# Kernel tuning notes

Hardware: AMD Instinct MI355X
Metric: run time of the kernel (lower is better)

## Reference

```python
import jax, jax.numpy as jnp
import numpy as np

N_NODES = 50000

def setup_inputs() -> dict:
    key = jax.random.key(0)
    ks = jax.random.split(key, 8)
    in_dim, hidden_dim, out_dim = 128, 128, 128
    n_edges = 800000
    features = jax.random.normal(ks[0], (N_NODES, in_dim), dtype=jnp.float32)
    src = jax.random.randint(ks[1], (n_edges,), 0, N_NODES, dtype=jnp.int64)
    dst = jax.random.randint(ks[2], (n_edges,), 0, N_NODES, dtype=jnp.int64)
    # nn.Linear params: weight [out,in], bias [out]
    W1 = jax.random.normal(ks[3], (hidden_dim, in_dim), dtype=jnp.float32) / np.sqrt(in_dim)
    b1 = jax.random.normal(ks[4], (hidden_dim,), dtype=jnp.float32) * 0.01
    W2 = jax.random.normal(ks[5], (out_dim, hidden_dim), dtype=jnp.float32) / np.sqrt(hidden_dim)
    b2 = jax.random.normal(ks[6], (out_dim,), dtype=jnp.float32) * 0.01
    return {"features": features, "src": src, "dst": dst,
            "W1": W1, "b1": b1, "W2": W2, "b2": b2}

def _mpnn_layer(feat, src, dst, W, b):
    # DGL copy_u + sum: message = feat[src], summed at dst nodes
    msgs = feat[src]                                  # [E, d] gather
    h_neigh = jax.ops.segment_sum(msgs, dst, num_segments=N_NODES)  # [N, d]
    return h_neigh @ W.T + b                          # dense linear

def reference(features, src, dst, W1, b1, W2, b2):
    h = _mpnn_layer(features, src, dst, W1, b1)
    h = jax.nn.relu(h)
    h = _mpnn_layer(h, src, dst, W2, b2)
    return h
```

## Files before the change

### kernel.cpp

```cpp
#include <hip/hip_runtime.h>


#define NDIM 128
#define SCAN_BS 512
#define BKT_SHIFT 8
#define BKT_NODES 256
#define TILE 4096
#define NBK_MAX 256

typedef __attribute__((ext_vector_type(8))) short bf16x8;
typedef __attribute__((ext_vector_type(4))) float f32x4;
typedef __attribute__((ext_vector_type(2))) float f32x2;

__device__ inline unsigned short f2bf_rne(float x) {
    unsigned u = __float_as_uint(x);
    unsigned lsb = (u >> 16) & 1u;
    u += 0x7fffu + lsb;
    return (unsigned short)(u >> 16);
}

__device__ inline unsigned pack_bf2(float lo, float hi) {
    return (unsigned)f2bf_rne(lo) | ((unsigned)f2bf_rne(hi) << 16);
}

__global__ __launch_bounds__(1024) void hist_convert(
        const int* __restrict__ dst, int* __restrict__ hist_g,
        int n_edges, int ntiles, int nbk,
        const float* __restrict__ feat, const float* __restrict__ W1,
        const float* __restrict__ W2,
        unsigned char* __restrict__ feat_f8,
        unsigned short* __restrict__ w1_bf,
        unsigned short* __restrict__ w2_bf, int n8) {
    __shared__ int lh[NBK_MAX];
    int t = threadIdx.x;
    if (blockIdx.x < (unsigned)ntiles) {
        int tblk = blockIdx.x;
        if (t < nbk) lh[t] = 0;
        __syncthreads();
        int e0 = tblk * TILE;
        int e1 = min(e0 + TILE, n_edges);
        for (int e = e0 + t; e < e1; e += 1024)
            atomicAdd(&lh[dst[e] >> BKT_SHIFT], 1);
        __syncthreads();
        if (t < nbk) hist_g[t * ntiles + tblk] = lh[t];
    } else {
        int i = (blockIdx.x - ntiles) * 1024 + t;
        if (i < n8) {
            const float4* p = reinterpret_cast<const float4*>(feat + (size_t)i * 8);
            float4 a = p[0], b = p[1];
            int w0 = __builtin_amdgcn_cvt_pk_fp8_f32(a.x, a.y, 0, false);
            w0 = __builtin_amdgcn_cvt_pk_fp8_f32(a.z, a.w, w0, true);
            int w1 = __builtin_amdgcn_cvt_pk_fp8_f32(b.x, b.y, 0, false);
            w1 = __builtin_amdgcn_cvt_pk_fp8_f32(b.z, b.w, w1, true);
            uint2 pk; pk.x = (unsigned)w0; pk.y = (unsigned)w1;
            *reinterpret_cast<uint2*>(feat_f8 + (size_t)i * 8) = pk;
        } else if (i < n8 + 4096) {
            int j = i - n8;
            const float* srcp = (j < 2048) ? W1 : W2;
            unsigned short* dstp = (j < 2048) ? w1_bf : w2_bf;
            int jj = j & 2047;
            const float4* p = reinterpret_cast<const float4*>(srcp + (size_t)jj * 8);
            float4 a = p[0], b = p[1];
            uint4 pk;
            pk.x = pack_bf2(a.x, a.y);
            pk.y = pack_bf2(a.z, a.w);
            pk.z = pack_bf2(b.x, b.y);
            pk.w = pack_bf2(b.z, b.w);
            *reinterpret_cast<uint4*>(dstp + (size_t)jj * 8) = pk;
        }
    }
}

__global__ __launch_bounds__(SCAN_BS) void scan_g_local(int* g, int* tsums, int n) {
    __shared__ int sh[SCAN_BS];
    int t = threadIdx.x;
    int i = blockIdx.x * SCAN_BS + t;
    int v = (i < n) ? g[i] : 0;
    sh[t] = v;
    __syncthreads();
    for (int off = 1; off < SCAN_BS; off <<= 1) {
        int u = (t >= off) ? sh[t - off] : 0;
        __syncthreads();
        sh[t] += u;
        __syncthreads();
    }
    if (i < n) g[i] = sh[t] - v;
    if (t == SCAN_BS - 1) tsums[blockIdx.x] = sh[t];
}

__global__ __launch_bounds__(SCAN_BS) void scan_g_apply2(int* g, const int* tsums,
                                                         int* bbase, int n,
                                                         int ntiles, int nbk) {
    __shared__ int part[128];
    int t = threadIdx.x;
    int b = blockIdx.x;
    if (t < 128) part[t] = (t < b) ? tsums[t] : 0;
    __syncthreads();
    for (int off = 64; off > 0; off >>= 1) {
        if (t < off) part[t] += part[t + off];
        __syncthreads();
    }
    int add = part[0];
    int i = b * SCAN_BS + t;
    if (i >= n) return;
    int r = g[i] + add;
    g[i] = r;
    if (i % ntiles == 0) {
        int bk = i / ntiles;
        if (bk < nbk) bbase[bk] = r;
    }
}

__global__ __launch_bounds__(128) void scan_blocksums(int* __restrict__ block_sums, int nb) {
    __shared__ int sh[128];
    int t = threadIdx.x;
    sh[t] = (t < nb) ? block_sums[t] : 0;
    __syncthreads();
    for (int off = 1; off < 128; off <<= 1) {
        int u = (t >= off) ? sh[t - off] : 0;
        __syncthreads();
        sh[t] += u;
        __syncthreads();
    }
    if (t < nb) block_sums[t] = sh[t];
}

__global__ __launch_bounds__(1024) void tile_scatter(const int* __restrict__ src,
                                                     const int* __restrict__ dst,
                                                     const int* __restrict__ hist_g,
                                                     unsigned* __restrict__ bdata,
                                                     int n_edges, int ntiles, int nbk) {
    __shared__ int lcur[NBK_MAX];
    __shared__ int lbase[NBK_MAX];
    __shared__ int gbase[NBK_MAX];
    __shared__ unsigned sorted[TILE];
    int tblk = blockIdx.x;
    int t = threadIdx.x;
    if (t < nbk) lcur[t] = 0;
    __syncthreads();
    int e0 = tblk * TILE;
    int e1 = min(e0 + TILE, n_edges);
    for (int e = e0 + t; e < e1; e += 1024)
        atomicAdd(&lcur[dst[e] >> BKT_SHIFT], 1);
    __syncthreads();
    if (t == 0) {
        int run = 0;
        for (int b = 0; b < nbk; ++b) { lbase[b] = run; run += lcur[b]; }
    }
    __syncthreads();
    if (t < nbk) {
        gbase[t] = hist_g[t * ntiles + tblk];
        lcur[t]  = lbase[t];
    }
    __syncthreads();
    for (int e = e0 + t; e < e1; e += 1024) {
        int d = dst[e];
        int s = src[e];
        int b = d >> BKT_SHIFT;
        int p = atomicAdd(&lcur[b], 1);
        sorted[p] = (unsigned)(s & 0xFFFF) | ((unsigned)(d & (BKT_NODES - 1)) << 16)
                  | ((unsigned)b << 24);
    }
    __syncthreads();
    int cnt = e1 - e0;
    for (int j = t; j < cnt; j += 1024) {
        unsigned pk = sorted[j];
        int b = pk >> 24;
        bdata[gbase[b] + (j - lbase[b])] = pk;
    }
}

__global__ __launch_bounds__(1024) void bucket_sort_rp(const int* __restrict__ bbase,
                                                       const unsigned* __restrict__ bdata,
                                                       int* __restrict__ row_ptr,
                                                       unsigned short* __restrict__ col,
                                                       int n_nodes, int n_edges, int nbk) {
    __shared__ int lcnt[BKT_NODES];
    __shared__ int lcur[BKT_NODES];
    int b = blockIdx.x;
    int t = threadIdx.x;
    int node0 = b << BKT_SHIFT;
    int nloc = min(BKT_NODES, n_nodes - node0);
    int base = bbase[b];
    int next = (b + 1 < nbk) ? bbase[b + 1] : n_edges;
    int cnt = next - base;
    if (t < BKT_NODES) lcnt[t] = 0;
    __syncthreads();
    for (int i = t; i < cnt; i += 1024)
        atomicAdd(&lcnt[(bdata[base + i] >> 16) & 255], 1);
    __syncthreads();
    int v = (t < BKT_NODES) ? lcnt[t] : 0;
    if (t < BKT_NODES) lcur[t] = v;
    __syncthreads();
    for (int off = 1; off < BKT_NODES; off <<= 1) {
        int u = (t >= off && t < BKT_NODES) ? lcur[t - off] : 0;
        __syncthreads();
        if (t < BKT_NODES) lcur[t] += u;
        __syncthreads();
    }
    int excl = lcur[t < BKT_NODES ? t : 0] - v;
    __syncthreads();
    if (t < BKT_NODES) lcur[t] = excl;
    if (t < nloc) row_ptr[node0 + t] = base + excl;
    if (b == nbk - 1 && t == 0) row_ptr[n_nodes] = n_edges;
    __syncthreads();
    for (int i = t; i < cnt; i += 1024) {
        unsigned pk = bdata[base + i];
        int pos = atomicAdd(&lcur[(pk >> 16) & 255], 1);
        col[base + pos] = (unsigned short)(pk & 0xFFFF);
    }
}

__global__ void aggregate_f8(const uint2* __restrict__ feat_f8,
                             const int* __restrict__ row_ptr,
                             const unsigned short* __restrict__ col,
                             uint4* __restrict__ out_bf,
                             int n_nodes) {
    int wid  = (blockIdx.x * blockDim.x + threadIdx.x) >> 6;
    int lane = threadIdx.x & 63;
    if (wid >= n_nodes) return;
    int sub = lane >> 4;
    int d   = lane & 15;
    int beg = row_ptr[wid];
    int end = row_ptr[wid + 1];
    float acc[8] = {0.f,0.f,0.f,0.f,0.f,0.f,0.f,0.f};

#define ACC_F8(aw) do {                                                     \
        f32x2 f_;                                                           \
        f_ = __builtin_amdgcn_cvt_pk_f32_fp8((int)(aw).x, false);           \
        acc[0] += f_.x; acc[1] += f_.y;                                     \
        f_ = __builtin_amdgcn_cvt_pk_f32_fp8((int)(aw).x, true);            \
        acc[2] += f_.x; acc[3] += f_.y;                                     \
        f_ = __builtin_amdgcn_cvt_pk_f32_fp8((int)(aw).y, false);           \
        acc[4] += f_.x; acc[5] += f_.y;                                     \
        f_ = __builtin_amdgcn_cvt_pk_f32_fp8((int)(aw).y, true);            \
        acc[6] += f_.x; acc[7] += f_.y;                                     \
    } while (0)

    int e = beg + sub;
    for (; e + 12 < end; e += 16) {
        int s0 = col[e];
        int s1 = col[e + 4];
        int s2 = col[e + 8];
        int s3 = col[e + 12];
        uint2 a0 = feat_f8[(size_t)s0 * 16 + d];
        uint2 a1 = feat_f8[(size_t)s1 * 16 + d];
        uint2 a2 = feat_f8[(size_t)s2 * 16 + d];
        uint2 a3 = feat_f8[(size_t)s3 * 16 + d];
        ACC_F8(a0); ACC_F8(a1); ACC_F8(a2); ACC_F8(a3);
    }
    for (; e + 4 < end; e += 8) {
        int s0 = col[e];
        int s1 = col[e + 4];
        uint2 a0 = feat_f8[(size_t)s0 * 16 + d];
        uint2 a1 = feat_f8[(size_t)s1 * 16 + d];
        ACC_F8(a0); ACC_F8(a1);
    }
    if (e < end) {
        uint2 a0 = feat_f8[(size_t)col[e] * 16 + d];
        ACC_F8(a0);
    }
#undef ACC_F8

#pragma unroll
    for (int j = 0; j < 8; ++j) {
        acc[j] += __shfl_xor(acc[j], 16, 64);
        acc[j] += __shfl_xor(acc[j], 32, 64);
    }
    if (sub == 0) {
        uint4 pk;
        pk.x = pack_bf2(acc[0], acc[1]);
        pk.y = pack_bf2(acc[2], acc[3]);
        pk.z = pack_bf2(acc[4], acc[5]);
        pk.w = pack_bf2(acc[6], acc[7]);
        out_bf[(size_t)wid * 16 + d] = pk;
    }
}

template <bool RELU, int OUTMODE>
__global__ __launch_bounds__(256) void linear_mfma(const unsigned short* __restrict__ h_bf,
                                                   const unsigned short* __restrict__ w_bf,
                                                   const float* __restrict__ bias,
                                                   float* __restrict__ out_f,
                                                   unsigned short* __restrict__ out_bf,
                                                   unsigned char* __restrict__ out_f8,
                                                   int n_nodes) {
    int t = threadIdx.x;
    int lane = t & 63;
    int wv = t >> 6;
    int r0 = blockIdx.x * 128 + wv * 32;
    int n1 = n_nodes - 1;
    int ra0 = min(r0 + (lane & 15), n1);
    int ra1 = min(r0 + 16 + (lane & 15), n1);
    int kb = (lane >> 4) * 8;
    int colb = lane & 15;

    f32x4 acc[2][8];
#pragma unroll
    for (int fr = 0; fr < 2; ++fr)
#pragma unroll
        for (int c = 0; c < 8; ++c)
            acc[fr][c] = (f32x4){0.f, 0.f, 0.f, 0.f};

#pragma unroll
    for (int kc = 0; kc < NDIM; kc += 32) {
        bf16x8 a0 = *reinterpret_cast<const bf16x8*>(h_bf + (size_t)ra0 * NDIM + kc + kb);
        bf16x8 a1 = *reinterpret_cast<const bf16x8*>(h_bf + (size_t)ra1 * NDIM + kc + kb);
#pragma unroll
        for (int c = 0; c < 8; ++c) {
            bf16x8 b = *reinterpret_cast<const bf16x8*>(
                w_bf + (size_t)(c * 16 + colb) * NDIM + kc + kb);
            acc[0][c] = __builtin_amdgcn_mfma_f32_16x16x32_bf16(a0, b, acc[0][c], 0, 0, 0);
            acc[1][c] = __builtin_amdgcn_mfma_f32_16x16x32_bf16(a1, b, acc[1][c], 0, 0, 0);
        }
    }

    int orow = (lane >> 4) * 4;
#pragma unroll
    for (int fr = 0; fr < 2; ++fr) {
#pragma unroll
        for (int c = 0; c < 8; ++c) {
            int colg = c * 16 + colb;
            float bv = bias[colg];
#pragma unroll
            for (int reg = 0; reg < 4; ++reg) {
                int row = r0 + fr * 16 + orow + reg;
                if (row >= n_nodes) continue;
                float v = acc[fr][c][reg] + bv;
                if (RELU) v = fmaxf(v, 0.f);
                if (OUTMODE == 2) {
                    int pk = __builtin_amdgcn_cvt_pk_fp8_f32(v, v, 0, false);
                    out_f8[(size_t)row * NDIM + colg] = (unsigned char)(pk & 0xFF);
                } else if (OUTMODE == 1) {
                    out_bf[(size_t)row * NDIM + colg] = f2bf_rne(v);
                } else {
                    out_f[(size_t)row * NDIM + colg] = v;
                }
            }
        }
    }
}

__global__ void hist_dst(const int* __restrict__ dst, int* __restrict__ counts, int n_edges) {
    int i = blockIdx.x * blockDim.x + threadIdx.x;
    if (i < n_edges) atomicAdd(&counts[dst[i]], 1);
}

__global__ __launch_bounds__(SCAN_BS) void scan_apply_fb(int* __restrict__ row_ptr,
                                                         int* __restrict__ cursor,
                                                         const int* __restrict__ block_sums,
                                                         int n, int nb) {
    int b = blockIdx.x;
    int i = b * SCAN_BS + threadIdx.x;
    int add = (b == 0) ? 0 : block_sums[b - 1];
    if (i < n) {
        int r = row_ptr[i] + add;
        row_ptr[i] = r;
        cursor[i]  = r;
    }
    if (i == 0) row_ptr[n] = block_sums[nb - 1];
}

__global__ void fill_csr(const int* __restrict__ src, const int* __restrict__ dst,
                         int* __restrict__ cursor, int* __restrict__ col, int n_edges) {
    int i = blockIdx.x * blockDim.x + threadIdx.x;
    if (i < n_edges) {
        int pos = atomicAdd(&cursor[dst[i]], 1);
        col[pos] = src[i];
    }
}

__global__ void transpose_w2(const float* __restrict__ W1, const float* __restrict__ W2,
                             float* __restrict__ WT1, float* __restrict__ WT2) {
    int tid = blockIdx.x * 256 + threadIdx.x;
    int which = tid >> 14;
    int t = tid & 16383;
    int o = t >> 7;
    int i = t & 127;
    if (which == 0) WT1[i * NDIM + o] = W1[o * NDIM + i];
    else            WT2[i * NDIM + o] = W2[o * NDIM + i];
}

__global__ void aggregate(const float* __restrict__ feat,
                          const int* __restrict__ row_ptr,
                          const int* __restrict__ col,
                          float* __restrict__ out, int n_nodes) {
    int wid  = (blockIdx.x * blockDim.x + threadIdx.x) >> 6;
    int lane = threadIdx.x & 63;
    if (wid >= n_nodes) return;
    int half = lane >> 5;
    int d4   = (lane & 31) << 2;
    int beg = row_ptr[wid];
    int end = row_ptr[wid + 1];
    float ax = 0.f, ay = 0.f, az = 0.f, aw = 0.f;
    int k = beg + half;
    for (; k < end; k += 2) {
        int s0 = col[k];
        float4 v0 = *reinterpret_cast<const float4*>(feat + (size_t)s0 * NDIM + d4);
        ax += v0.x; ay += v0.y; az += v0.z; aw += v0.w;
    }
    ax += __shfl(ax, lane ^ 32, 64);
    ay += __shfl(ay, lane ^ 32, 64);
    az += __shfl(az, lane ^ 32, 64);
    aw += __shfl(aw, lane ^ 32, 64);
    if (half == 0) {
        float4 r; r.x = ax; r.y = ay; r.z = az; r.w = aw;
        *reinterpret_cast<float4*>(out + (size_t)wid * NDIM + d4) = r;
    }
}

template <bool RELU>
__global__ void linear_k(const float* __restrict__ h, const float* __restrict__ WT,
                         const float* __restrict__ bias, float* __restrict__ out,
                         int n_nodes) {
    int tid = blockIdx.x * blockDim.x + threadIdx.x;
    int row = tid >> 5;
    if (row >= n_nodes) return;
    int c4 = (tid & 31) << 2;
    const float4* h4 = reinterpret_cast<const float4*>(h + (size_t)row * NDIM);
    float4 acc = make_float4(0.f, 0.f, 0.f, 0.f);
#pragma unroll 8
    for (int k4 = 0; k4 < 32; ++k4) {
        float4 hv = h4[k4];
        const float* wt = WT + (k4 * 4) * NDIM + c4;
        float4 w0 = *reinterpret_cast<const float4*>(wt);
        float4 w1 = *reinterpret_cast<const float4*>(wt + NDIM);
        float4 w2 = *reinterpret_cast<const float4*>(wt + 2 * NDIM);
        float4 w3 = *reinterpret_cast<const float4*>(wt + 3 * NDIM);
        acc.x = fmaf(hv.x, w0.x, acc.x); acc.y = fmaf(hv.x, w0.y, acc.y);
        acc.z = fmaf(hv.x, w0.z, acc.z); acc.w = fmaf(hv.x, w0.w, acc.w);
        acc.x = fmaf(hv.y, w1.x, acc.x); acc.y = fmaf(hv.y, w1.y, acc.y);
        acc.z = fmaf(hv.y, w1.z, acc.z); acc.w = fmaf(hv.y, w1.w, acc.w);
        acc.x = fmaf(hv.z, w2.x, acc.x); acc.y = fmaf(hv.z, w2.y, acc.y);
        acc.z = fmaf(hv.z, w2.z, acc.z); acc.w = fmaf(hv.z, w2.w, acc.w);
        acc.x = fmaf(hv.w, w3.x, acc.x); acc.y = fmaf(hv.w, w3.y, acc.y);
        acc.z = fmaf(hv.w, w3.z, acc.z); acc.w = fmaf(hv.w, w3.w, acc.w);
    }
    float4 bv = *reinterpret_cast<const float4*>(bias + c4);
    acc.x += bv.x; acc.y += bv.y; acc.z += bv.z; acc.w += bv.w;
    if (RELU) {
        acc.x = fmaxf(acc.x, 0.f); acc.y = fmaxf(acc.y, 0.f);
        acc.z = fmaxf(acc.z, 0.f); acc.w = fmaxf(acc.w, 0.f);
    }
    *reinterpret_cast<float4*>(out + (size_t)row * NDIM + c4) = acc;
}

extern "C" void kernel_launch(void* const* d_in, const int* in_sizes, int n_in,
                              void* d_out, int out_size, void* d_ws, size_t ws_size,
                              hipStream_t stream) {
    const float* features = (const float*)d_in[0];
    const int*   src      = (const int*)d_in[1];
    const int*   dst      = (const int*)d_in[2];
    const float* W1       = (const float*)d_in[3];
    const float* b1       = (const float*)d_in[4];
    const float* W2       = (const float*)d_in[5];
    const float* b2       = (const float*)d_in[6];
    float* out = (float*)d_out;

    int n_nodes = in_sizes[0] / NDIM;
    int n_edges = in_sizes[1];
    int nbk = (n_nodes + BKT_NODES - 1) >> BKT_SHIFT;
    int ntiles = (n_edges + TILE - 1) / TILE;
    int rp_pad = ((n_nodes + 1 + 3) / 4) * 4;

    char* base = (char*)d_ws;
    unsigned short* hneigh_bf = (unsigned short*)base;
    unsigned short* w1_bf  = hneigh_bf + (size_t)n_nodes * NDIM;
    unsigned short* w2_bf  = w1_bf + NDIM * NDIM;
    int*   row_ptr = (int*)(w2_bf + NDIM * NDIM);
    int*   col_i   = row_ptr + rp_pad;
    unsigned short* col_us = (unsigned short*)col_i;
    unsigned char* feat_f8 = (unsigned char*)(col_i + n_edges);
    int*      hist_g = (int*)(feat_f8 + (((size_t)n_nodes * NDIM + 15) & ~15ull));
    int*      bbase  = hist_g + (size_t)nbk * ntiles;
    int*      tsums  = bbase + ((nbk + 3) / 4) * 4;
    unsigned* bdata  = (unsigned*)(tsums + 128);
    float* WT1    = (float*)(bdata + n_edges);
    float* WT2    = WT1 + NDIM * NDIM;
    int*   counts = (int*)(WT2 + NDIM * NDIM);
    int*   cursor = counts + n_nodes;
    float* hneigh_f = (float*)(cursor + n_nodes);

    size_t needed_fast = (char*)(bdata + n_edges) - base;
    size_t needed_fb   = (char*)(hneigh_f + (size_t)n_nodes * NDIM) - base;

    unsigned char* h1_f8 = (unsigned char*)d_out;

    int eb = (n_edges + 255) / 256;
    int nscan = nbk * ntiles;
    int nsb = (nscan + SCAN_BS - 1) / SCAN_BS;
    bool fast = (ws_size >= needed_fast) && (n_nodes <= 65536)
              && (nbk <= NBK_MAX) && (nsb <= 128);

    if (fast) {
        int n8 = n_nodes * (NDIM / 8);
        int cvt_blocks = (n8 + 4096 + 1023) / 1024;

        hist_convert<<<ntiles + cvt_blocks, 1024, 0, stream>>>(
            dst, hist_g, n_edges, ntiles, nbk,
            features, W1, W2, feat_f8, w1_bf, w2_bf, n8);
        scan_g_local<<<nsb, SCAN_BS, 0, stream>>>(hist_g, tsums, nscan);
        scan_g_apply2<<<nsb, SCAN_BS, 0, stream>>>(hist_g, tsums, bbase, nscan, ntiles, nbk);
        tile_scatter<<<ntiles, 1024, 0, stream>>>(src, dst, hist_g, bdata,
                                                  n_edges, ntiles, nbk);
        bucket_sort_rp<<<nbk, 1024, 0, stream>>>(bbase, bdata, row_ptr, col_us,
                                                 n_nodes, n_edges, nbk);

        int ab = (int)(((long)n_nodes * 64 + 255) / 256);
        int lb = (n_nodes + 127) / 128;

        aggregate_f8<<<ab, 256, 0, stream>>>((const uint2*)feat_f8, row_ptr, col_us,
                                             (uint4*)hneigh_bf, n_nodes);
        linear_mfma<true, 2><<<lb, 256, 0, stream>>>(hneigh_bf, w1_bf, b1,
                                                     nullptr, nullptr, h1_f8, n_nodes);
        aggregate_f8<<<ab, 256, 0, stream>>>((const uint2*)h1_f8, row_ptr, col_us,
                                             (uint4*)hneigh_bf, n_nodes);
        linear_mfma<false, 0><<<lb, 256, 0, stream>>>(hneigh_bf, w2_bf, b2,
                                                      out, nullptr, nullptr, n_nodes);
    } else if (ws_size >= needed_fb) {
        transpose_w2<<<128, 256, 0, stream>>>(W1, W2, WT1, WT2);
        hipMemsetAsync(counts, 0, (size_t)n_nodes * sizeof(int), stream);
        hist_dst<<<eb, 256, 0, stream>>>(dst, counts, n_edges);
        int nb = (n_nodes + SCAN_BS - 1) / SCAN_BS;
        scan_g_local<<<nb, SCAN_BS, 0, stream>>>(counts, tsums, n_nodes);
        scan_blocksums<<<1, 128, 0, stream>>>(tsums, nb);
        scan_apply_fb<<<nb, SCAN_BS, 0, stream>>>(counts, cursor, tsums, n_nodes, nb);
        hipMemcpyAsync(row_ptr, counts, (size_t)(n_nodes + 1) * sizeof(int),
                       hipMemcpyDeviceToDevice, stream);
        fill_csr<<<eb, 256, 0, stream>>>(src, dst, cursor, col_i, n_edges);

        int ab = (int)(((long)n_nodes * 64 + 255) / 256);
        int lk = (n_nodes * 32 + 255) / 256;
        aggregate<<<ab, 256, 0, stream>>>(features, row_ptr, col_i, hneigh_f, n_nodes);
        linear_k<true><<<lk, 256, 0, stream>>>(hneigh_f, WT1, b1, out, n_nodes);
        aggregate<<<ab, 256, 0, stream>>>(out, row_ptr, col_i, hneigh_f, n_nodes);
        linear_k<false><<<lk, 256, 0, stream>>>(hneigh_f, WT2, b2, out, n_nodes);
    }
}
```

Baseline: 117.6 us.

## Merge two-pass histogram scan into single-pass decoupled lookback scan

Replaces the scan_g_local and scan_g_apply2 pair with one kernel in which each block publishes its aggregate through an acquire/release flag and spins on the aggregates of earlier blocks, removing one kernel launch. The flags are zeroed inside hist_convert. tile_scatter's serial single-thread prefix over buckets becomes a parallel shared-memory Hillis-Steele scan. The unused bf16 output mode of linear_mfma is dropped. The spin-wait assumes all earlier blocks are resident, which holds only for a small grid (nsb is at most 128).

```diff
diff --git a/kernel.cpp b/kernel.cpp
--- a/kernel.cpp
+++ b/kernel.cpp
@@ -30,9 +30,11 @@
         const float* __restrict__ W2,
         unsigned char* __restrict__ feat_f8,
         unsigned short* __restrict__ w1_bf,
-        unsigned short* __restrict__ w2_bf, int n8) {
+        unsigned short* __restrict__ w2_bf, int n8,
+        int* __restrict__ agg_flags) {
     __shared__ int lh[NBK_MAX];
     int t = threadIdx.x;
+    if (blockIdx.x == 0 && t < 128) agg_flags[t] = 0;
     if (blockIdx.x < (unsigned)ntiles) {
         int tblk = blockIdx.x;
         if (t < nbk) lh[t] = 0;
@@ -71,6 +73,50 @@
     }
 }
 
+__global__ __launch_bounds__(SCAN_BS) void scan_g_lookback(
+        int* g, int* agg, int* bbase, int n, int ntiles, int nbk) {
+    __shared__ int sh[SCAN_BS];
+    __shared__ int part[128];
+    int t = threadIdx.x;
+    int b = blockIdx.x;
+    int i = b * SCAN_BS + t;
+    int v = (i < n) ? g[i] : 0;
+    sh[t] = v;
+    __syncthreads();
+    for (int off = 1; off < SCAN_BS; off <<= 1) {
+        int u = (t >= off) ? sh[t - off] : 0;
+        __syncthreads();
+        sh[t] += u;
+        __syncthreads();
+    }
+    if (t == 0)
+        __hip_atomic_store(&agg[b], sh[SCAN_BS - 1] + 1,
+                           __ATOMIC_RELEASE, __HIP_MEMORY_SCOPE_AGENT);
+    if (t < 128) {
+        int val = 0;
+        if (t < b) {
+            while ((val = __hip_atomic_load(&agg[t], __ATOMIC_ACQUIRE,
+                                            __HIP_MEMORY_SCOPE_AGENT)) == 0) {}
+            val -= 1;
+        }
+        part[t] = val;
+    }
+    __syncthreads();
+    for (int off = 64; off > 0; off >>= 1) {
+        if (t < off) part[t] += part[t + off];
+        __syncthreads();
+    }
+    int add = part[0];
+    if (i < n) {
+        int r = sh[t] - v + add;
+        g[i] = r;
+        if (i % ntiles == 0) {
+            int bk = i / ntiles;
+            if (bk < nbk) bbase[bk] = r;
+        }
+    }
+}
+
 __global__ __launch_bounds__(SCAN_BS) void scan_g_local(int* g, int* tsums, int n) {
     __shared__ int sh[SCAN_BS];
     int t = threadIdx.x;
@@ -86,29 +132,6 @@
     }
     if (i < n) g[i] = sh[t] - v;
     if (t == SCAN_BS - 1) tsums[blockIdx.x] = sh[t];
-}
-
-__global__ __launch_bounds__(SCAN_BS) void scan_g_apply2(int* g, const int* tsums,
-                                                         int* bbase, int n,
-                                                         int ntiles, int nbk) {
-    __shared__ int part[128];
-    int t = threadIdx.x;
-    int b = blockIdx.x;
-    if (t < 128) part[t] = (t < b) ? tsums[t] : 0;
-    __syncthreads();
-    for (int off = 64; off > 0; off >>= 1) {
-        if (t < off) part[t] += part[t + off];
-        __syncthreads();
-    }
-    int add = part[0];
-    int i = b * SCAN_BS + t;
-    if (i >= n) return;
-    int r = g[i] + add;
-    g[i] = r;
-    if (i % ntiles == 0) {
-        int bk = i / ntiles;
-        if (bk < nbk) bbase[bk] = r;
-    }
 }
 
 __global__ __launch_bounds__(128) void scan_blocksums(int* __restrict__ block_sums, int nb) {
@@ -143,10 +166,15 @@
     for (int e = e0 + t; e < e1; e += 1024)
         atomicAdd(&lcur[dst[e] >> BKT_SHIFT], 1);
     __syncthreads();
-    if (t == 0) {
-        int run = 0;
-        for (int b = 0; b < nbk; ++b) { lbase[b] = run; run += lcur[b]; }
-    }
+    if (t < nbk) lbase[t] = lcur[t];
+    __syncthreads();
+    for (int off = 1; off < NBK_MAX; off <<= 1) {
+        int u = (t >= off && t < nbk) ? lbase[t - off] : 0;
+        __syncthreads();
+        if (t < nbk) lbase[t] += u;
+        __syncthreads();
+    }
+    if (t < nbk) lbase[t] -= lcur[t];
     __syncthreads();
     if (t < nbk) {
         gbase[t] = hist_g[t * ntiles + tblk];
@@ -282,7 +310,6 @@
                                                    const unsigned short* __restrict__ w_bf,
                                                    const float* __restrict__ bias,
                                                    float* __restrict__ out_f,
-                                                   unsigned short* __restrict__ out_bf,
                                                    unsigned char* __restrict__ out_f8,
                                                    int n_nodes) {
     int t = threadIdx.x;
@@ -331,8 +358,6 @@
                 if (OUTMODE == 2) {
                     int pk = __builtin_amdgcn_cvt_pk_fp8_f32(v, v, 0, false);
                     out_f8[(size_t)row * NDIM + colg] = (unsigned char)(pk & 0xFF);
-                } else if (OUTMODE == 1) {
-                    out_bf[(size_t)row * NDIM + colg] = f2bf_rne(v);
                 } else {
                     out_f[(size_t)row * NDIM + colg] = v;
                 }
@@ -498,9 +523,9 @@
 
         hist_convert<<<ntiles + cvt_blocks, 1024, 0, stream>>>(
             dst, hist_g, n_edges, ntiles, nbk,
-            features, W1, W2, feat_f8, w1_bf, w2_bf, n8);
-        scan_g_local<<<nsb, SCAN_BS, 0, stream>>>(hist_g, tsums, nscan);
-        scan_g_apply2<<<nsb, SCAN_BS, 0, stream>>>(hist_g, tsums, bbase, nscan, ntiles, nbk);
+            features, W1, W2, feat_f8, w1_bf, w2_bf, n8, tsums);
+        scan_g_lookback<<<nsb, SCAN_BS, 0, stream>>>(hist_g, tsums, bbase,
+                                                     nscan, ntiles, nbk);
         tile_scatter<<<ntiles, 1024, 0, stream>>>(src, dst, hist_g, bdata,
                                                   n_edges, ntiles, nbk);
         bucket_sort_rp<<<nbk, 1024, 0, stream>>>(bbase, bdata, row_ptr, col_us,
@@ -512,11 +537,11 @@
         aggregate_f8<<<ab, 256, 0, stream>>>((const uint2*)feat_f8, row_ptr, col_us,
                                              (uint4*)hneigh_bf, n_nodes);
         linear_mfma<true, 2><<<lb, 256, 0, stream>>>(hneigh_bf, w1_bf, b1,
-                                                     nullptr, nullptr, h1_f8, n_nodes);
+                                                     nullptr, h1_f8, n_nodes);
         aggregate_f8<<<ab, 256, 0, stream>>>((const uint2*)h1_f8, row_ptr, col_us,
                                              (uint4*)hneigh_bf, n_nodes);
         linear_mfma<false, 0><<<lb, 256, 0, stream>>>(hneigh_bf, w2_bf, b2,
-                                                      out, nullptr, nullptr, n_nodes);
+                                                      out, nullptr, n_nodes);
     } else if (ws_size >= needed_fb) {
         transpose_w2<<<128, 256, 0, stream>>>(W1, W2, WT1, WT2);
         hipMemsetAsync(counts, 0, (size_t)n_nodes * sizeof(int), stream);
```

New measurement: 115.8 us. Within noise of the previous version (-1.6%).
